# Kernel tuning notes

Measured on AMD Instinct MI355X. Metric: run time of the kernel, lower is better.

Reference implementation:

```python
import jax, jax.numpy as jnp
import numpy as np

D_MODEL = 768
NUM_HEADS = 12
HEAD_DIM = D_MODEL // NUM_HEADS


def setup_inputs() -> dict:
    key = jax.random.key(0)
    ks = jax.random.split(key, 9)
    B, S = 2, 2048
    s = 1.0 / np.sqrt(D_MODEL)
    x = jax.random.normal(ks[0], (B, S, D_MODEL), dtype=jnp.float32)
    Wq = jax.random.normal(ks[1], (D_MODEL, D_MODEL), dtype=jnp.float32) * s
    Wk = jax.random.normal(ks[2], (D_MODEL, D_MODEL), dtype=jnp.float32) * s
    Wv = jax.random.normal(ks[3], (D_MODEL, D_MODEL), dtype=jnp.float32) * s
    Wo = jax.random.normal(ks[4], (D_MODEL, D_MODEL), dtype=jnp.float32) * s
    bq = jax.random.normal(ks[5], (D_MODEL,), dtype=jnp.float32) * 0.01
    bk = jax.random.normal(ks[6], (D_MODEL,), dtype=jnp.float32) * 0.01
    bv = jax.random.normal(ks[7], (D_MODEL,), dtype=jnp.float32) * 0.01
    bo = jax.random.normal(ks[8], (D_MODEL,), dtype=jnp.float32) * 0.01
    return {"x": x, "Wq": Wq, "bq": bq, "Wk": Wk, "bk": bk,
            "Wv": Wv, "bv": bv, "Wo": Wo, "bo": bo}


def reference(x, Wq, bq, Wk, bk, Wv, bv, Wo, bo):
    B, S, _ = x.shape
    # projections; reshape to [B, H, S, Dh]
    def split_heads(t):
        return t.reshape(B, S, NUM_HEADS, HEAD_DIM).transpose(0, 2, 1, 3)
    q = split_heads(x @ Wq + bq)
    k = split_heads(x @ Wk + bk)
    v = split_heads(x @ Wv + bv)
    scale = 1.0 / np.sqrt(HEAD_DIM)
    scores = jnp.einsum("bhqd,bhkd->bhqk", q, k) * scale  # [B,H,S,S]
    attn = jax.nn.softmax(scores, axis=-1)
    # dropout p=0.0 (eval) -> identity
    ctx = jnp.einsum("bhqk,bhkd->bhqd", attn, v)
    ctx = ctx.transpose(0, 2, 1, 3).reshape(B, S, D_MODEL)
    return ctx @ Wo + bo
```

## Files before the change

### kernel.cpp

```cpp
#include <hip/hip_runtime.h>
#include <hip/hip_bf16.h>
#include <hip/hip_fp16.h>

#define D_MODEL 768
#define NHEADS  12
#define HD      64
#define BATCH   2
#define SEQ     2048
#define NTOK    (BATCH*SEQ)
#define NX      ((size_t)NTOK * D_MODEL)
#define NW      ((size_t)D_MODEL * D_MODEL)
#define SC_LOG2 0.18033688f

typedef __attribute__((ext_vector_type(8))) short    short8;
typedef __attribute__((ext_vector_type(8))) _Float16 half8;
typedef __attribute__((ext_vector_type(4))) float    f32x4;

__device__ __forceinline__ float bf2f(short s) {
    union { unsigned u; float f; } c;
    c.u = ((unsigned)(unsigned short)s) << 16;
    return c.f;
}
__device__ __forceinline__ short f2bf(float f) {
    __hip_bfloat16 h = __float2bfloat16(f);
    return *(short*)&h;
}

#ifdef __has_builtin
#if __has_builtin(__builtin_amdgcn_global_load_lds)
#define HAS_GLD 1
#endif
#endif
#ifdef HAS_GLD
#define GLD16(gp, lp) __builtin_amdgcn_global_load_lds( \
    (const __attribute__((address_space(1))) void*)(gp), \
    (__attribute__((address_space(3))) void*)(lp), 16, 0, 0)
#endif

__global__ void detect_and_bias(const short* __restrict__ x, int* __restrict__ flag,
                                const void* __restrict__ b0, const void* __restrict__ b1,
                                const void* __restrict__ b2, const void* __restrict__ b3,
                                short* __restrict__ dst)
{
    __shared__ int red[256];
    const int tid = threadIdx.x;
    int maxe = 0;
    for (int i = tid; i < 4096; i += 256) {
        int e = ((unsigned short)x[i] >> 7) & 0xFF;
        maxe = max(maxe, e);
    }
    red[tid] = maxe;
    __syncthreads();
    for (int s = 128; s > 0; s >>= 1) {
        if (tid < s) red[tid] = max(red[tid], red[tid + s]);
        __syncthreads();
    }
    const bool isf = (red[0] > 140);
    if (tid == 0) *flag = isf ? 1 : 0;
    const void* srcs[4] = { b0, b1, b2, b3 };
    for (int z = 0; z < 4; ++z) {
        const float sc = (z == 0) ? SC_LOG2 : 1.0f;
        for (int i = tid; i < D_MODEL; i += 256) {
            float v = isf ? ((const float*)srcs[z])[i] : bf2f(((const short*)srcs[z])[i]);
            dst[z * D_MODEL + i] = f2bf(v * sc);
        }
    }
}

__global__ void conv_x4(const void* __restrict__ src, short* __restrict__ dst,
                        int n4, const int* __restrict__ flag) {
    const int i = blockIdx.x * 256 + threadIdx.x;
    if (i >= n4) return;
    if (*flag) {
        float4 f = ((const float4*)src)[i];
        short4 o = { f2bf(f.x), f2bf(f.y), f2bf(f.z), f2bf(f.w) };
        ((short4*)dst)[i] = o;
    } else {
        ((short4*)dst)[i] = ((const short4*)src)[i];
    }
}

__global__ __launch_bounds__(256) void conv_wt(const void* __restrict__ w0,
                                               const void* __restrict__ w1,
                                               const void* __restrict__ w2,
                                               const void* __restrict__ w3,
                                               short* __restrict__ wt,
                                               const int* __restrict__ flag)
{
    __shared__ float T[64][65];
    const int z = blockIdx.z;
    const void* src = (z == 0) ? w0 : (z == 1) ? w1 : (z == 2) ? w2 : w3;
    const float sc = (z == 0) ? SC_LOG2 : 1.0f;
    const int k0 = blockIdx.x * 64, n0 = blockIdx.y * 64;
    const int a = threadIdx.x & 15, b = threadIdx.x >> 4;
    const bool isf = (*flag != 0);
#pragma unroll
    for (int u = 0; u < 4; ++u) {
        const int kr = (b & 3) + 4 * u + 16 * (b >> 2);
        if (isf) {
            float4 f = *(const float4*)((const float*)src + (size_t)(k0 + kr) * D_MODEL + n0 + a * 4);
            T[kr][a*4+0] = f.x; T[kr][a*4+1] = f.y; T[kr][a*4+2] = f.z; T[kr][a*4+3] = f.w;
        } else {
            short4 s = *(const short4*)((const short*)src + (size_t)(k0 + kr) * D_MODEL + n0 + a * 4);
            T[kr][a*4+0] = bf2f(s.x); T[kr][a*4+1] = bf2f(s.y); T[kr][a*4+2] = bf2f(s.z); T[kr][a*4+3] = bf2f(s.w);
        }
    }
    __syncthreads();
#pragma unroll
    for (int u = 0; u < 4; ++u) {
        const int nr = (b & 3) + 4 * u + 16 * (b >> 2);
        short4 o = { f2bf(T[a*4+0][nr] * sc), f2bf(T[a*4+1][nr] * sc),
                     f2bf(T[a*4+2][nr] * sc), f2bf(T[a*4+3][nr] * sc) };
        *(short4*)(wt + (size_t)z * NW + (size_t)(n0 + nr) * D_MODEL + k0 + a * 4) = o;
    }
}

__global__ __launch_bounds__(256) void qkv_gemm(const short* __restrict__ X,
                                                const short* __restrict__ Wt,
                                                const short* __restrict__ bias,
                                                short* __restrict__ qb,
                                                short* __restrict__ kb,
                                                _Float16* __restrict__ Vt)
{
    __shared__ __align__(16) char shbuf[32768];
    short* Als = (short*)shbuf;
    short* Bls = (short*)(shbuf + 16384);
    _Float16* T = (_Float16*)shbuf;

    const int tid = threadIdx.x;
    const int wave = tid >> 6, lane = tid & 63;
    const int quad = lane >> 4, l16 = lane & 15;
    const int wm = wave & 1, wn = wave >> 1;
    const int m0 = blockIdx.x * 128;
    const int ng = blockIdx.y * 128;

    f32x4 acc[4][4];
#pragma unroll
    for (int nt = 0; nt < 4; ++nt) {
        const float bv = bf2f(bias[ng + wn*64 + nt*16 + l16]);
#pragma unroll
        for (int mt = 0; mt < 4; ++mt) acc[mt][nt] = (f32x4){bv, bv, bv, bv};
    }

    const int row = tid >> 2, ch = (tid & 3) * 8;
#ifdef HAS_GLD
#define QSTAGE(buf, k0) do { \
        GLD16(X  + (size_t)(m0 + row)      * D_MODEL + (k0) + ch, &Als[(buf)*4096 + tid*8]); \
        GLD16(X  + (size_t)(m0 + 64 + row) * D_MODEL + (k0) + ch, &Als[(buf)*4096 + 2048 + tid*8]); \
        GLD16(Wt + (size_t)(ng + row)      * D_MODEL + (k0) + ch, &Bls[(buf)*4096 + tid*8]); \
        GLD16(Wt + (size_t)(ng + 64 + row) * D_MODEL + (k0) + ch, &Bls[(buf)*4096 + 2048 + tid*8]); \
    } while (0)
#else
#define QSTAGE(buf, k0) do { \
        short8 r0 = *(const short8*)(X  + (size_t)(m0 + row)      * D_MODEL + (k0) + ch); \
        short8 r1 = *(const short8*)(X  + (size_t)(m0 + 64 + row) * D_MODEL + (k0) + ch); \
        short8 r2 = *(const short8*)(Wt + (size_t)(ng + row)      * D_MODEL + (k0) + ch); \
        short8 r3 = *(const short8*)(Wt + (size_t)(ng + 64 + row) * D_MODEL + (k0) + ch); \
        *(short8*)&Als[(buf)*4096 + tid*8] = r0;  *(short8*)&Als[(buf)*4096 + 2048 + tid*8] = r1; \
        *(short8*)&Bls[(buf)*4096 + tid*8] = r2;  *(short8*)&Bls[(buf)*4096 + 2048 + tid*8] = r3; \
    } while (0)
#endif

    QSTAGE(0, 0);
    __syncthreads();

    for (int ks = 0; ks < 24; ++ks) {
        const int cur = ks & 1;
        if (ks + 1 < 24) QSTAGE(cur ^ 1, (ks + 1) * 32);

        short8 a[4], b[4];
#pragma unroll
        for (int mt = 0; mt < 4; ++mt)
            a[mt] = *(const short8*)&Als[cur*4096 + (wm*64 + mt*16 + l16) * 32 + quad*8];
#pragma unroll
        for (int nt = 0; nt < 4; ++nt)
            b[nt] = *(const short8*)&Bls[cur*4096 + (wn*64 + nt*16 + l16) * 32 + quad*8];
#pragma unroll
        for (int mt = 0; mt < 4; ++mt)
#pragma unroll
        for (int nt = 0; nt < 4; ++nt)
            acc[mt][nt] = __builtin_amdgcn_mfma_f32_16x16x32_bf16(a[mt], b[nt], acc[mt][nt], 0, 0, 0);

        __syncthreads();
    }
#undef QSTAGE

    const int seg = blockIdx.y / 6;
    if (seg < 2) {
        short* out = seg ? kb : qb;
        const int nl = ng - seg * 768;
#pragma unroll
        for (int mt = 0; mt < 4; ++mt)
#pragma unroll
        for (int nt = 0; nt < 4; ++nt) {
            const int n = nl + wn*64 + nt*16 + l16;
#pragma unroll
            for (int r = 0; r < 4; ++r) {
                const int m = m0 + wm*64 + mt*16 + quad*4 + r;
                out[(size_t)m * D_MODEL + n] = f2bf(acc[mt][nt][r]);
            }
        }
    } else {
        const int batch = m0 >> 11, tokb = m0 & (SEQ - 1);
        for (int pass = 0; pass < 2; ++pass) {
            if (wn == pass) {
#pragma unroll
                for (int nt = 0; nt < 4; ++nt) {
                    const int dim_l = nt*16 + l16;
#pragma unroll
                    for (int mt = 0; mt < 4; ++mt) {
                        const int tok_l = wm*64 + mt*16 + quad*4;
                        union { _Float16 h4[4]; int2 v; } u;
#pragma unroll
                        for (int r = 0; r < 4; ++r) u.h4[r] = (_Float16)acc[mt][nt][r];
                        *(int2*)&T[dim_l * 136 + tok_l] = u.v;
                    }
                }
            }
            __syncthreads();
#pragma unroll
            for (int u = 0; u < 4; ++u) {
                const int slot = tid + u * 256;
                const int drow = slot >> 4, chk = slot & 15;
                int4 val = *(const int4*)&T[drow * 136 + chk * 8];
                const int dim_g = ng - 1536 + pass*64 + drow;
                const int h = dim_g >> 6, d = dim_g & 63;
                *(int4*)(Vt + ((size_t)(batch * NHEADS + h) * HD + d) * SEQ + tokb + chk*8) = val;
            }
            if (pass == 0) __syncthreads();
        }
    }
}

__global__ __launch_bounds__(256) void out_gemm(const short* __restrict__ X,
                                                const short* __restrict__ Wt,
                                                const short* __restrict__ bias,
                                                void* __restrict__ outv,
                                                const int* __restrict__ flag)
{
    __shared__ short Als[2][2048];
    __shared__ short Bls[2][2048];

    const int tid = threadIdx.x;
    const int wave = tid >> 6, lane = tid & 63;
    const int quad = lane >> 4, l16 = lane & 15;
    const int m0 = blockIdx.x * 64;
    const int n0 = blockIdx.y * 64;

    f32x4 acc[4];
#pragma unroll
    for (int nt = 0; nt < 4; ++nt) {
        const float bv = bf2f(bias[n0 + nt*16 + l16]);
        acc[nt] = (f32x4){bv, bv, bv, bv};
    }

    const int row = tid >> 2, ch = (tid & 3) * 8;
#ifdef HAS_GLD
#define OSTAGE(buf, k0) do { \
        GLD16(X  + (size_t)(m0 + row) * D_MODEL + (k0) + ch, &Als[buf][tid*8]); \
        GLD16(Wt + (size_t)(n0 + row) * D_MODEL + (k0) + ch, &Bls[buf][tid*8]); \
    } while (0)
#else
#define OSTAGE(buf, k0) do { \
        short8 r0 = *(const short8*)(X  + (size_t)(m0 + row) * D_MODEL + (k0) + ch); \
        short8 r1 = *(const short8*)(Wt + (size_t)(n0 + row) * D_MODEL + (k0) + ch); \
        *(short8*)&Als[buf][tid*8] = r0; \
        *(short8*)&Bls[buf][tid*8] = r1; \
    } while (0)
#endif

    OSTAGE(0, 0);
    __syncthreads();

    for (int ks = 0; ks < 24; ++ks) {
        const int cur = ks & 1;
        if (ks + 1 < 24) OSTAGE(cur ^ 1, (ks + 1) * 32);

        short8 a = *(const short8*)&Als[cur][(wave*16 + l16) * 32 + quad*8];
#pragma unroll
        for (int nt = 0; nt < 4; ++nt) {
            short8 b = *(const short8*)&Bls[cur][(nt*16 + l16) * 32 + quad*8];
            acc[nt] = __builtin_amdgcn_mfma_f32_16x16x32_bf16(a, b, acc[nt], 0, 0, 0);
        }
        __syncthreads();
    }
#undef OSTAGE

    const bool outf32 = (*flag != 0);
#pragma unroll
    for (int nt = 0; nt < 4; ++nt) {
        const int n = n0 + nt*16 + l16;
#pragma unroll
        for (int r = 0; r < 4; ++r) {
            const int m = m0 + wave*16 + quad*4 + r;
            const size_t idx = (size_t)m * D_MODEL + n;
            if (outf32) ((float*)outv)[idx] = acc[nt][r];
            else        ((short*)outv)[idx] = f2bf(acc[nt][r]);
        }
    }
}

#define PSTR 72
__global__ __launch_bounds__(256) void attn_mfma(const short* __restrict__ q,
                                                 const short* __restrict__ k,
                                                 const _Float16* __restrict__ Vt,
                                                 short* __restrict__ ctx)
{
    __shared__ short    Kls[2][64 * 64];
    __shared__ _Float16 Vls[2][64 * 64];
    __shared__ _Float16 Pls[4][16 * PSTR];

    const int tid  = threadIdx.x;
    const int wave = tid >> 6, lane = tid & 63;
    const int quad = lane >> 4, l16 = lane & 15;
    const int bh = blockIdx.y;
    const int b = bh / NHEADS, h = bh % NHEADS;
    const size_t bS = (size_t)b * SEQ;
    const int q0 = blockIdx.x * 64;
    const int myq = q0 + wave * 16 + l16;

    short8 qf[2];
#pragma unroll
    for (int k0h = 0; k0h < 2; ++k0h)
        qf[k0h] = *(const short8*)(q + (bS + myq) * D_MODEL + h*HD + k0h*32 + quad*8);

    half8 ones;
#pragma unroll
    for (int j = 0; j < 8; ++j) ones[j] = (_Float16)1.0f;

    const int s0 = tid, s1 = tid + 256;
    const int kr0 = s0 >> 3, kc0 = (s0 & 7) ^ (kr0 & 7);
    const int kr1 = s1 >> 3, kc1 = (s1 & 7) ^ (kr1 & 7);
    const short*    kg0 = k  + (bS + kr0) * D_MODEL + h*HD + kc0*8;
    const short*    kg1 = k  + (bS + kr1) * D_MODEL + h*HD + kc1*8;
    const _Float16* vg0 = Vt + ((size_t)bh * HD + kr0) * SEQ + kc0*8;
    const _Float16* vg1 = Vt + ((size_t)bh * HD + kr1) * SEQ + kc1*8;

#ifdef HAS_GLD
#define STAGE(buf, j0) do { \
        GLD16(kg0 + (size_t)(j0) * D_MODEL, &Kls[buf][s0 * 8]); \
        GLD16(kg1 + (size_t)(j0) * D_MODEL, &Kls[buf][s1 * 8]); \
        GLD16(vg0 + (j0),                   &Vls[buf][s0 * 8]); \
        GLD16(vg1 + (j0),                   &Vls[buf][s1 * 8]); \
    } while (0)
#else
#define STAGE(buf, j0) do { \
        short8 a_ = *(const short8*)(kg0 + (size_t)(j0) * D_MODEL); \
        short8 b_ = *(const short8*)(kg1 + (size_t)(j0) * D_MODEL); \
        half8  c_ = *(const half8*)(vg0 + (j0)); \
        half8  d_ = *(const half8*)(vg1 + (j0)); \
        *(short8*)&Kls[buf][s0 * 8] = a_;  *(short8*)&Kls[buf][s1 * 8] = b_; \
        *(half8*)&Vls[buf][s0 * 8] = c_;   *(half8*)&Vls[buf][s1 * 8] = d_; \
    } while (0)
#endif

    float m_ = -1e30f;
    f32x4 lacc = (f32x4){0.f, 0.f, 0.f, 0.f};
    f32x4 o[4];
#pragma unroll
    for (int t = 0; t < 4; ++t) o[t] = (f32x4){0.f, 0.f, 0.f, 0.f};

    STAGE(0, 0);
    __syncthreads();

    for (int jt = 0; jt < SEQ / 64; ++jt) {
        const int cur = jt & 1;
        if (jt + 1 < SEQ / 64) STAGE(cur ^ 1, (jt + 1) * 64);

        f32x4 s4[4];
#pragma unroll
        for (int t = 0; t < 4; ++t) s4[t] = (f32x4){0.f, 0.f, 0.f, 0.f};
#pragma unroll
        for (int k0h = 0; k0h < 2; ++k0h)
#pragma unroll
        for (int t = 0; t < 4; ++t) {
            const int krow = t*16 + l16;
            short8 kf = *(const short8*)&Kls[cur][krow*64 + (((k0h*4 + quad) ^ (krow & 7)) * 8)];
            s4[t] = __builtin_amdgcn_mfma_f32_16x16x32_bf16(kf, qf[k0h], s4[t], 0, 0, 0);
        }

        float mx = s4[0][0];
#pragma unroll
        for (int t = 0; t < 4; ++t)
#pragma unroll
        for (int r = 0; r < 4; ++r) mx = fmaxf(mx, s4[t][r]);
#pragma unroll
        for (int d = 1; d < 64; d <<= 1) mx = fmaxf(mx, __shfl_xor(mx, d));
        const float mn = fmaxf(m_, mx);
        if (__builtin_amdgcn_readfirstlane((int)(mn > m_))) {
            const float al = exp2f(m_ - mn);
#pragma unroll
            for (int t = 0; t < 4; ++t) {
                o[t][0] *= al; o[t][1] *= al; o[t][2] *= al; o[t][3] *= al;
            }
            lacc[0] *= al; lacc[1] *= al; lacc[2] *= al; lacc[3] *= al;
            m_ = mn;
        }

#pragma unroll
        for (int t = 0; t < 4; ++t) {
            union { _Float16 h4[4]; int2 v; } u4;
#pragma unroll
            for (int r = 0; r < 4; ++r) u4.h4[r] = (_Float16)exp2f(s4[t][r] - mn);
            *(int2*)&Pls[wave][l16 * PSTR + t*16 + quad*4] = u4.v;
        }

#pragma unroll
        for (int k0h = 0; k0h < 2; ++k0h) {
            half8 pf = *(half8*)&Pls[wave][l16 * PSTR + k0h*32 + quad*8];
            lacc = __builtin_amdgcn_mfma_f32_16x16x32_f16(ones, pf, lacc, 0, 0, 0);
#pragma unroll
            for (int t = 0; t < 4; ++t) {
                const int vrow = t*16 + l16;
                half8 vf = *(const half8*)&Vls[cur][vrow*64 + (((k0h*4 + quad) ^ (vrow & 7)) * 8)];
                o[t] = __builtin_amdgcn_mfma_f32_16x16x32_f16(vf, pf, o[t], 0, 0, 0);
            }
        }

        __syncthreads();
    }

    const float inv = 1.0f / lacc[0];
    const size_t rowp = (bS + myq) * D_MODEL + h*HD;
#pragma unroll
    for (int t = 0; t < 4; ++t) {
        union { short s4v[4]; int2 v; } u4;
#pragma unroll
        for (int r = 0; r < 4; ++r) u4.s4v[r] = f2bf(o[t][r] * inv);
        *(int2*)(ctx + rowp + t*16 + quad*4) = u4.v;
    }
#undef STAGE
}

extern "C" void kernel_launch(void* const* d_in, const int* in_sizes, int n_in,
                              void* d_out, int out_size, void* d_ws, size_t ws_size,
                              hipStream_t stream)
{
    int* flag = (int*)d_ws;
    short* xc = (short*)((char*)d_ws + 64);
    short* Wt = xc + NX;
    short* bc = Wt + 4 * NW;
    short* qb = bc + 4 * D_MODEL;
    short* kb = qb + NX;
    _Float16* Vt = (_Float16*)(kb + NX);
    short* cb = (short*)(Vt + NX);

    detect_and_bias<<<1, 256, 0, stream>>>((const short*)d_in[0], flag,
                                           d_in[2], d_in[4], d_in[6], d_in[8], bc);
    conv_x4<<<(int)(NX/4 + 255) / 256, 256, 0, stream>>>(d_in[0], xc, (int)(NX/4), flag);
    conv_wt<<<dim3(12, 12, 4), 256, 0, stream>>>(d_in[1], d_in[3], d_in[5], d_in[7], Wt, flag);

    qkv_gemm<<<dim3(NTOK/128, 2304/128), 256, 0, stream>>>(xc, Wt, bc, qb, kb, Vt);

    attn_mfma<<<dim3(SEQ/64, BATCH*NHEADS), 256, 0, stream>>>(qb, kb, Vt, cb);

    out_gemm<<<dim3(NTOK/64, D_MODEL/64), 256, 0, stream>>>(cb, Wt + 3*NW, bc + 3*D_MODEL, d_out, flag);
}
```

Before: 204.5 us.

## Fuse input conversion kernels and remap attention blocks for XCD locality

```diff
diff --git a/kernel.cpp b/kernel.cpp
--- a/kernel.cpp
+++ b/kernel.cpp
@@ -37,81 +37,83 @@
     (__attribute__((address_space(3))) void*)(lp), 16, 0, 0)
 #endif
 
-__global__ void detect_and_bias(const short* __restrict__ x, int* __restrict__ flag,
-                                const void* __restrict__ b0, const void* __restrict__ b1,
-                                const void* __restrict__ b2, const void* __restrict__ b3,
-                                short* __restrict__ dst)
+__global__ __launch_bounds__(256) void fused_conv(
+        const void* __restrict__ xin,
+        const void* __restrict__ w0, const void* __restrict__ w1,
+        const void* __restrict__ w2, const void* __restrict__ w3,
+        const void* __restrict__ b0, const void* __restrict__ b1,
+        const void* __restrict__ b2, const void* __restrict__ b3,
+        short* __restrict__ xc, short* __restrict__ wt,
+        short* __restrict__ bc, int* __restrict__ flag)
 {
     __shared__ int red[256];
+    __shared__ float T[64][65];
     const int tid = threadIdx.x;
-    int maxe = 0;
-    for (int i = tid; i < 4096; i += 256) {
-        int e = ((unsigned short)x[i] >> 7) & 0xFF;
-        maxe = max(maxe, e);
-    }
-    red[tid] = maxe;
-    __syncthreads();
-    for (int s = 128; s > 0; s >>= 1) {
-        if (tid < s) red[tid] = max(red[tid], red[tid + s]);
+    const int F = blockIdx.x;
+
+    {
+        const short* xs = (const short*)xin;
+        int maxe = 0;
+#pragma unroll
+        for (int u = 0; u < 16; ++u) {
+            int e = ((unsigned short)xs[tid * 16 + u] >> 7) & 0xFF;
+            maxe = max(maxe, e);
+        }
+        red[tid] = maxe;
         __syncthreads();
+        for (int s = 128; s > 0; s >>= 1) {
+            if (tid < s) red[tid] = max(red[tid], red[tid + s]);
+            __syncthreads();
+        }
     }
     const bool isf = (red[0] > 140);
-    if (tid == 0) *flag = isf ? 1 : 0;
-    const void* srcs[4] = { b0, b1, b2, b3 };
-    for (int z = 0; z < 4; ++z) {
+
+    if (F < 3072) {
+        const int i = F * 256 + tid;
+        if (isf) {
+            float4 f = ((const float4*)xin)[i];
+            short4 o = { f2bf(f.x), f2bf(f.y), f2bf(f.z), f2bf(f.w) };
+            ((short4*)xc)[i] = o;
+        } else {
+            ((short4*)xc)[i] = ((const short4*)xin)[i];
+        }
+    } else if (F < 3648) {
+        const int G = F - 3072;
+        const int z = G / 144, rr = G % 144;
+        const int k0 = (rr % 12) * 64, n0 = (rr / 12) * 64;
+        const void* src = (z == 0) ? w0 : (z == 1) ? w1 : (z == 2) ? w2 : w3;
         const float sc = (z == 0) ? SC_LOG2 : 1.0f;
-        for (int i = tid; i < D_MODEL; i += 256) {
-            float v = isf ? ((const float*)srcs[z])[i] : bf2f(((const short*)srcs[z])[i]);
-            dst[z * D_MODEL + i] = f2bf(v * sc);
-        }
-    }
-}
-
-__global__ void conv_x4(const void* __restrict__ src, short* __restrict__ dst,
-                        int n4, const int* __restrict__ flag) {
-    const int i = blockIdx.x * 256 + threadIdx.x;
-    if (i >= n4) return;
-    if (*flag) {
-        float4 f = ((const float4*)src)[i];
-        short4 o = { f2bf(f.x), f2bf(f.y), f2bf(f.z), f2bf(f.w) };
-        ((short4*)dst)[i] = o;
+        const int la = tid & 15, lb = tid >> 4;
+#pragma unroll
+        for (int u = 0; u < 4; ++u) {
+            const int kr = (lb & 3) + 4 * u + 16 * (lb >> 2);
+            if (isf) {
+                float4 f = *(const float4*)((const float*)src + (size_t)(k0 + kr) * D_MODEL + n0 + la * 4);
+                T[kr][la*4+0] = f.x; T[kr][la*4+1] = f.y; T[kr][la*4+2] = f.z; T[kr][la*4+3] = f.w;
+            } else {
+                short4 s = *(const short4*)((const short*)src + (size_t)(k0 + kr) * D_MODEL + n0 + la * 4);
+                T[kr][la*4+0] = bf2f(s.x); T[kr][la*4+1] = bf2f(s.y);
+                T[kr][la*4+2] = bf2f(s.z); T[kr][la*4+3] = bf2f(s.w);
+            }
+        }
+        __syncthreads();
+#pragma unroll
+        for (int u = 0; u < 4; ++u) {
+            const int nr = (lb & 3) + 4 * u + 16 * (lb >> 2);
+            short4 o = { f2bf(T[la*4+0][nr] * sc), f2bf(T[la*4+1][nr] * sc),
+                         f2bf(T[la*4+2][nr] * sc), f2bf(T[la*4+3][nr] * sc) };
+            *(short4*)(wt + (size_t)z * NW + (size_t)(n0 + nr) * D_MODEL + k0 + la * 4) = o;
+        }
     } else {
-        ((short4*)dst)[i] = ((const short4*)src)[i];
-    }
-}
-
-__global__ __launch_bounds__(256) void conv_wt(const void* __restrict__ w0,
-                                               const void* __restrict__ w1,
-                                               const void* __restrict__ w2,
-                                               const void* __restrict__ w3,
-                                               short* __restrict__ wt,
-                                               const int* __restrict__ flag)
-{
-    __shared__ float T[64][65];
-    const int z = blockIdx.z;
-    const void* src = (z == 0) ? w0 : (z == 1) ? w1 : (z == 2) ? w2 : w3;
-    const float sc = (z == 0) ? SC_LOG2 : 1.0f;
-    const int k0 = blockIdx.x * 64, n0 = blockIdx.y * 64;
-    const int a = threadIdx.x & 15, b = threadIdx.x >> 4;
-    const bool isf = (*flag != 0);
-#pragma unroll
-    for (int u = 0; u < 4; ++u) {
-        const int kr = (b & 3) + 4 * u + 16 * (b >> 2);
-        if (isf) {
-            float4 f = *(const float4*)((const float*)src + (size_t)(k0 + kr) * D_MODEL + n0 + a * 4);
-            T[kr][a*4+0] = f.x; T[kr][a*4+1] = f.y; T[kr][a*4+2] = f.z; T[kr][a*4+3] = f.w;
-        } else {
-            short4 s = *(const short4*)((const short*)src + (size_t)(k0 + kr) * D_MODEL + n0 + a * 4);
-            T[kr][a*4+0] = bf2f(s.x); T[kr][a*4+1] = bf2f(s.y); T[kr][a*4+2] = bf2f(s.z); T[kr][a*4+3] = bf2f(s.w);
-        }
-    }
-    __syncthreads();
-#pragma unroll
-    for (int u = 0; u < 4; ++u) {
-        const int nr = (b & 3) + 4 * u + 16 * (b >> 2);
-        short4 o = { f2bf(T[a*4+0][nr] * sc), f2bf(T[a*4+1][nr] * sc),
-                     f2bf(T[a*4+2][nr] * sc), f2bf(T[a*4+3][nr] * sc) };
-        *(short4*)(wt + (size_t)z * NW + (size_t)(n0 + nr) * D_MODEL + k0 + a * 4) = o;
+        if (tid == 0) *flag = isf ? 1 : 0;
+        const void* srcs[4] = { b0, b1, b2, b3 };
+        for (int z = 0; z < 4; ++z) {
+            const float sc = (z == 0) ? SC_LOG2 : 1.0f;
+            for (int i = tid; i < D_MODEL; i += 256) {
+                float v = isf ? ((const float*)srcs[z])[i] : bf2f(((const short*)srcs[z])[i]);
+                bc[z * D_MODEL + i] = f2bf(v * sc);
+            }
+        }
     }
 }
 
@@ -300,7 +302,6 @@
     }
 }
 
-#define PSTR 72
 __global__ __launch_bounds__(256) void attn_mfma(const short* __restrict__ q,
                                                  const short* __restrict__ k,
                                                  const _Float16* __restrict__ Vt,
@@ -308,15 +309,18 @@
 {
     __shared__ short    Kls[2][64 * 64];
     __shared__ _Float16 Vls[2][64 * 64];
-    __shared__ _Float16 Pls[4][16 * PSTR];
+    __shared__ _Float16 Pls[4][16 * 64];
 
     const int tid  = threadIdx.x;
     const int wave = tid >> 6, lane = tid & 63;
     const int quad = lane >> 4, l16 = lane & 15;
-    const int bh = blockIdx.y;
+
+    const int F = blockIdx.x;
+    const int xcd = F & 7, slot = F >> 3;
+    const int bh = xcd * 3 + (slot >> 5);
+    const int q0 = (slot & 31) * 64;
     const int b = bh / NHEADS, h = bh % NHEADS;
     const size_t bS = (size_t)b * SEQ;
-    const int q0 = blockIdx.x * 64;
     const int myq = q0 + wave * 16 + l16;
 
     short8 qf[2];
@@ -402,12 +406,14 @@
             union { _Float16 h4[4]; int2 v; } u4;
 #pragma unroll
             for (int r = 0; r < 4; ++r) u4.h4[r] = (_Float16)exp2f(s4[t][r] - mn);
-            *(int2*)&Pls[wave][l16 * PSTR + t*16 + quad*4] = u4.v;
+            const int c = (t*2 + (quad >> 1)) ^ (l16 & 7);
+            *(int2*)&Pls[wave][l16*64 + c*8 + (quad & 1)*4] = u4.v;
         }
 
 #pragma unroll
         for (int k0h = 0; k0h < 2; ++k0h) {
-            half8 pf = *(half8*)&Pls[wave][l16 * PSTR + k0h*32 + quad*8];
+            const int pc = (k0h*4 + quad) ^ (l16 & 7);
+            half8 pf = *(half8*)&Pls[wave][l16*64 + pc*8];
             lacc = __builtin_amdgcn_mfma_f32_16x16x32_f16(ones, pf, lacc, 0, 0, 0);
 #pragma unroll
             for (int t = 0; t < 4; ++t) {
@@ -445,14 +451,14 @@
     _Float16* Vt = (_Float16*)(kb + NX);
     short* cb = (short*)(Vt + NX);
 
-    detect_and_bias<<<1, 256, 0, stream>>>((const short*)d_in[0], flag,
-                                           d_in[2], d_in[4], d_in[6], d_in[8], bc);
-    conv_x4<<<(int)(NX/4 + 255) / 256, 256, 0, stream>>>(d_in[0], xc, (int)(NX/4), flag);
-    conv_wt<<<dim3(12, 12, 4), 256, 0, stream>>>(d_in[1], d_in[3], d_in[5], d_in[7], Wt, flag);
+    fused_conv<<<3649, 256, 0, stream>>>(d_in[0],
+                                         d_in[1], d_in[3], d_in[5], d_in[7],
+                                         d_in[2], d_in[4], d_in[6], d_in[8],
+                                         xc, Wt, bc, flag);
 
     qkv_gemm<<<dim3(NTOK/128, 2304/128), 256, 0, stream>>>(xc, Wt, bc, qb, kb, Vt);
 
-    attn_mfma<<<dim3(SEQ/64, BATCH*NHEADS), 256, 0, stream>>>(qb, kb, Vt, cb);
+    attn_mfma<<<768, 256, 0, stream>>>(qb, kb, Vt, cb);
 
     out_gemm<<<dim3(NTOK/64, D_MODEL/64), 256, 0, stream>>>(cb, Wt + 3*NW, bc + 3*D_MODEL, d_out, flag);
 }
```

Result: faster. 195.1 us (-4.6%).
